# Kernel optimization log

Measured on AMD Instinct MI355X. Metric: run time of the kernel, lower is better.

## Reference

```python
import jax, jax.numpy as jnp
import numpy as np

B, D, H = 8192, 1024, 4096


def setup_inputs() -> dict:
    key = jax.random.key(0)
    ks = jax.random.split(key, 8)
    s_in = 1.0 / np.sqrt(D)
    s_hid = 1.0 / np.sqrt(H)
    return {
        "x": jax.random.normal(ks[0], (B, D), dtype=jnp.float32),
        "Wr": jax.random.normal(ks[1], (D, 1), dtype=jnp.float32) * s_in,
        "br": jnp.zeros((1,), dtype=jnp.float32),
        "W1l": jax.random.normal(ks[2], (D, H), dtype=jnp.float32) * s_in,
        "b1l": jnp.zeros((H,), dtype=jnp.float32),
        "W2l": jax.random.normal(ks[3], (H, D), dtype=jnp.float32) * s_hid,
        "b2l": jnp.zeros((D,), dtype=jnp.float32),
        "W1r": jax.random.normal(ks[4], (D, H), dtype=jnp.float32) * s_in,
        "b1r": jnp.zeros((H,), dtype=jnp.float32),
        "W2r": jax.random.normal(ks[5], (H, D), dtype=jnp.float32) * s_hid,
        "b2r": jnp.zeros((D,), dtype=jnp.float32),
    }


def _expert(x, W1, b1, W2, b2):
    # 2-layer MLP expert: [B, D] -> [B, H] -> [B, D]
    h = jax.nn.relu(x @ W1 + b1)
    return h @ W2 + b2


def reference(x, Wr, br, W1l, b1l, W2l, b2l, W1r, b1r, W2r, b2r):
    # Router probability p in (0, 1): [B, 1]
    p = jax.nn.sigmoid(x @ Wr + br)
    left = _expert(x, W1l, b1l, W2l, b2l)   # [B, D]
    right = _expert(x, W1r, b1r, W2r, b2r)  # [B, D]
    # soft_decision branch: convex combination of children per sample
    return p * left + (1.0 - p) * right
```

## Files before the change

### kernel.cpp

```cpp
#include <hip/hip_runtime.h>
#include <hip/hip_bf16.h>
#include <cstdint>
#include <cstddef>

#define B_DIM  8192
#define D_DIM  1024
#define H_DIM  4096
#define H2_DIM 8192

using bf16 = __hip_bfloat16;
typedef __attribute__((ext_vector_type(8))) short bf16x8;
typedef __attribute__((ext_vector_type(4))) float f32x4;

__global__ __launch_bounds__(256) void cast_f32_to_bf16(const float* __restrict__ in,
                                                        bf16* __restrict__ out, int n_vec8) {
    int i = blockIdx.x * 256 + threadIdx.x;
    if (i >= n_vec8) return;
    const float4* src = reinterpret_cast<const float4*>(in) + (size_t)i * 2;
    float4 a = src[0], b = src[1];
    union { bf16 h[8]; int4 u; } r;
    r.h[0] = __float2bfloat16(a.x); r.h[1] = __float2bfloat16(a.y);
    r.h[2] = __float2bfloat16(a.z); r.h[3] = __float2bfloat16(a.w);
    r.h[4] = __float2bfloat16(b.x); r.h[5] = __float2bfloat16(b.y);
    r.h[6] = __float2bfloat16(b.z); r.h[7] = __float2bfloat16(b.w);
    reinterpret_cast<int4*>(out)[i] = r.u;
}

__global__ __launch_bounds__(256) void router_kernel(const float* __restrict__ x,
                                                     const float* __restrict__ Wr,
                                                     const float* __restrict__ br,
                                                     float* __restrict__ p) {
    int wave = threadIdx.x >> 6, lane = threadIdx.x & 63;
    int row = blockIdx.x * 4 + wave;
    const float* xr = x + (size_t)row * D_DIM;
    float sum = 0.f;
#pragma unroll
    for (int it = 0; it < 4; ++it) {
        int k = it * 256 + lane * 4;
        float4 xv = *reinterpret_cast<const float4*>(xr + k);
        float4 wv = *reinterpret_cast<const float4*>(Wr + k);
        sum += xv.x * wv.x + xv.y * wv.y + xv.z * wv.z + xv.w * wv.w;
    }
#pragma unroll
    for (int off = 32; off >= 1; off >>= 1) sum += __shfl_down(sum, off, 64);
    if (lane == 0) p[row] = 1.f / (1.f + expf(-(sum + br[0])));
}

__global__ __launch_bounds__(256) void transpose_cast_kernel(const float* __restrict__ src,
                                                             int R, int C,
                                                             bf16* __restrict__ dst, int dstLD) {
    __shared__ float tile[32][33];
    int c0 = blockIdx.x * 32, r0 = blockIdx.y * 32;
    int tx = threadIdx.x & 31, ty = threadIdx.x >> 5;
#pragma unroll
    for (int i = 0; i < 32; i += 8)
        tile[ty + i][tx] = src[(size_t)(r0 + ty + i) * C + c0 + tx];
    __syncthreads();
#pragma unroll
    for (int i = 0; i < 32; i += 8)
        dst[(size_t)(c0 + ty + i) * dstLD + r0 + tx] = __float2bfloat16(tile[tx][ty + i]);
}

template<int NBH, int EPI>
__global__ __launch_bounds__(512, 2) void gemm8(const bf16* __restrict__ A,
                                                const bf16* __restrict__ Bt,
                                                void* __restrict__ Cout,
                                                int N, int K, int NT, int nbx,
                                                const float* __restrict__ p,
                                                const float* __restrict__ bias_l,
                                                const float* __restrict__ bias_r) {
    constexpr int NREP   = 2 * NBH;
    constexpr int HALF_B = 16384;
    constexpr int BUFB   = (2 + NBH) * HALF_B;
    constexpr int BN     = NBH * 128;
    __shared__ __align__(16) char lds[2 * BUFB];

    const int tid  = threadIdx.x;
    const int wid  = tid >> 6, lane = tid & 63;
    const int wr   = wid >> 2, wcn = wid & 3;

    const int cpx     = (int)gridDim.x >> 3;
    const int logical = ((int)blockIdx.x & 7) * cpx + ((int)blockIdx.x >> 3);
    const int by = logical / nbx, bx = logical - by * nbx;
    const int bm = by * 256, bn = bx * BN;

    const int      srow = tid >> 3;
    const uint32_t coff = (uint32_t)(((tid & 7) ^ (srow & 7)) << 3);
    uint32_t offA[2][2], offB[NBH][2];
#pragma unroll
    for (int h = 0; h < 2; ++h)
#pragma unroll
        for (int r = 0; r < 2; ++r)
            offA[h][r] = (uint32_t)(bm + h * 128 + r * 64 + srow) * (uint32_t)K + coff;
#pragma unroll
    for (int h = 0; h < NBH; ++h)
#pragma unroll
        for (int r = 0; r < 2; ++r)
            offB[h][r] = (uint32_t)(bn + h * 128 + r * 64 + srow) * (uint32_t)K + coff;

#define STAGE(PAR, KT) do {                                                                  \
    const uint32_t k64_ = (uint32_t)(KT) * 64u;                                              \
    _Pragma("unroll") for (int h_ = 0; h_ < 2; ++h_)                                         \
      _Pragma("unroll") for (int r_ = 0; r_ < 2; ++r_)                                       \
        __builtin_amdgcn_global_load_lds(                                                    \
          (const __attribute__((address_space(1))) uint32_t*)(A + (size_t)(offA[h_][r_] + k64_)), \
          (__attribute__((address_space(3))) uint32_t*)(lds + (PAR)*BUFB + h_*HALF_B + r_*8192 + wid*1024), \
          16, 0, 0);                                                                         \
    _Pragma("unroll") for (int h_ = 0; h_ < NBH; ++h_)                                       \
      _Pragma("unroll") for (int r_ = 0; r_ < 2; ++r_)                                       \
        __builtin_amdgcn_global_load_lds(                                                    \
          (const __attribute__((address_space(1))) uint32_t*)(Bt + (size_t)(offB[h_][r_] + k64_)), \
          (__attribute__((address_space(3))) uint32_t*)(lds + (PAR)*BUFB + (2+h_)*HALF_B + r_*8192 + wid*1024), \
          16, 0, 0);                                                                         \
} while (0)

    const int      lrow  = lane & 15, kg = lane >> 4;
    const uint32_t s0    = (uint32_t)((kg ^ (lrow & 7)) << 4);
    const uint32_t baseA = (uint32_t)(wr * HALF_B + lrow * 128) + s0;
    const int      colt0 = wcn * (NREP * 16);
    const uint32_t baseB = (uint32_t)((2 + (colt0 >> 7)) * HALF_B + ((colt0 & 127) + lrow) * 128) + s0;

#define RD(off) (*reinterpret_cast<const bf16x8*>(lds + (off)))

    f32x4 acc[8][NREP];
#pragma unroll
    for (int m = 0; m < 8; ++m)
#pragma unroll
        for (int n = 0; n < NREP; ++n) acc[m][n] = (f32x4){0.f, 0.f, 0.f, 0.f};

#define VM_WAIT_STEADY() do {                                              \
    if (NBH == 2) asm volatile("s_waitcnt vmcnt(8)" ::: "memory");         \
    else          asm volatile("s_waitcnt vmcnt(6)" ::: "memory");         \
} while (0)

#define TILE_BODY(PAR, KT, STG, LASTT) do {                                                   \
    bf16x8 bf_[NREP][2], af_[4][2];                                                           \
    _Pragma("unroll") for (int n = 0; n < NREP; ++n)                                          \
      _Pragma("unroll") for (int kk = 0; kk < 2; ++kk)                                        \
        bf_[n][kk] = RD(((uint32_t)((PAR)*BUFB) + baseB + (uint32_t)(n*2048)) ^ (uint32_t)(kk*64)); \
    _Pragma("unroll") for (int m = 0; m < 4; ++m)                                             \
      _Pragma("unroll") for (int kk = 0; kk < 2; ++kk)                                        \
        af_[m][kk] = RD(((uint32_t)((PAR)*BUFB) + baseA + (uint32_t)(m*2048)) ^ (uint32_t)(kk*64)); \
    __builtin_amdgcn_s_setprio(1);                                                            \
    _Pragma("unroll") for (int m = 0; m < 4; ++m)                                             \
      _Pragma("unroll") for (int n = 0; n < NREP; ++n)                                        \
        _Pragma("unroll") for (int kk = 0; kk < 2; ++kk)                                      \
          acc[m][n] = __builtin_amdgcn_mfma_f32_16x16x32_bf16(af_[m][kk], bf_[n][kk], acc[m][n], 0, 0, 0); \
    __builtin_amdgcn_s_setprio(0);                                                            \
    _Pragma("unroll") for (int m = 0; m < 4; ++m)                                             \
      _Pragma("unroll") for (int kk = 0; kk < 2; ++kk)                                        \
        af_[m][kk] = RD(((uint32_t)((PAR)*BUFB) + baseA + (uint32_t)(8192 + m*2048)) ^ (uint32_t)(kk*64)); \
    __builtin_amdgcn_sched_barrier(0);                                                        \
    asm volatile("s_waitcnt lgkmcnt(0)" ::: "memory");                                        \
    __builtin_amdgcn_sched_barrier(0);                                                        \
    __builtin_amdgcn_s_barrier();                                                             \
    __builtin_amdgcn_sched_barrier(0);                                                        \
    if (STG) { STAGE(PAR, (KT) + 2); }                                                        \
    __builtin_amdgcn_sched_barrier(0);                                                        \
    __builtin_amdgcn_s_setprio(1);                                                            \
    _Pragma("unroll") for (int m = 0; m < 4; ++m)                                             \
      _Pragma("unroll") for (int n = 0; n < NREP; ++n)                                        \
        _Pragma("unroll") for (int kk = 0; kk < 2; ++kk)                                      \
          acc[4+m][n] = __builtin_amdgcn_mfma_f32_16x16x32_bf16(af_[m][kk], bf_[n][kk], acc[4+m][n], 0, 0, 0); \
    __builtin_amdgcn_s_setprio(0);                                                            \
    if (!(LASTT)) {                                                                           \
      __builtin_amdgcn_sched_barrier(0);                                                      \
      if (STG) { VM_WAIT_STEADY(); }                                                          \
      else     { asm volatile("s_waitcnt vmcnt(0)" ::: "memory"); }                           \
      __builtin_amdgcn_sched_barrier(0);                                                      \
      __builtin_amdgcn_s_barrier();                                                           \
      __builtin_amdgcn_sched_barrier(0);                                                      \
    }                                                                                         \
} while (0)

    STAGE(0, 0);
    STAGE(1, 1);
    VM_WAIT_STEADY();
    __builtin_amdgcn_sched_barrier(0);
    __builtin_amdgcn_s_barrier();
    __builtin_amdgcn_sched_barrier(0);

    int kt = 0;
    for (; kt < NT - 2; kt += 2) {
        TILE_BODY(0, kt,     true, false);
        TILE_BODY(1, kt + 1, true, false);
    }
    TILE_BODY(0, NT - 2, false, false);
    TILE_BODY(1, NT - 1, false, true);

    const int crow0 = bm + wr * 128 + (kg << 2);
    const int ccol0 = bn + wcn * (NREP * 16) + lrow;

    if (EPI == 1) {
        bf16* __restrict__ Ho = (bf16*)Cout;
#pragma unroll
        for (int n = 0; n < NREP; ++n) {
            const int col = ccol0 + n * 16;
            const bool left = col < H_DIM;
            const float bias = left ? bias_l[col] : bias_r[col - H_DIM];
#pragma unroll
            for (int m = 0; m < 8; ++m) {
#pragma unroll
                for (int j = 0; j < 4; ++j) {
                    const int row = crow0 + m * 16 + j;
                    const float pw = p[row];
                    const float scale = left ? pw : 1.f - pw;
                    const float v = fmaxf(acc[m][n][j] + bias, 0.f) * scale;
                    Ho[(size_t)row * N + col] = __float2bfloat16(v);
                }
            }
        }
    } else {
        float* __restrict__ Co = (float*)Cout;
#pragma unroll
        for (int n = 0; n < NREP; ++n) {
            const int col = ccol0 + n * 16;
            const float bl = bias_l[col];
            const float brr = bias_r[col];
#pragma unroll
            for (int m = 0; m < 8; ++m) {
#pragma unroll
                for (int j = 0; j < 4; ++j) {
                    const int row = crow0 + m * 16 + j;
                    const float pw = p[row];
                    Co[(size_t)row * N + col] = acc[m][n][j] + pw * bl + (1.f - pw) * brr;
                }
            }
        }
    }
#undef TILE_BODY
#undef VM_WAIT_STEADY
#undef RD
#undef STAGE
}

extern "C" void kernel_launch(void* const* d_in, const int* in_sizes, int n_in,
                              void* d_out, int out_size, void* d_ws, size_t ws_size,
                              hipStream_t stream) {
    const float* x   = (const float*)d_in[0];
    const float* Wr  = (const float*)d_in[1];
    const float* br  = (const float*)d_in[2];
    const float* W1l = (const float*)d_in[3];
    const float* b1l = (const float*)d_in[4];
    const float* W2l = (const float*)d_in[5];
    const float* b2l = (const float*)d_in[6];
    const float* W1r = (const float*)d_in[7];
    const float* b1r = (const float*)d_in[8];
    const float* W2r = (const float*)d_in[9];
    const float* b2r = (const float*)d_in[10];
    float* out = (float*)d_out;

    char* ws = (char*)d_ws;
    bf16*  x_bf = (bf16*)(ws);
    bf16*  W1t  = (bf16*)(ws + (size_t)(16u << 20));
    bf16*  hbuf = (bf16*)(ws + (size_t)(32u << 20));
    float* pbuf = (float*)(ws + (size_t)(160u << 20));
    bf16*  W2t  = x_bf;

    cast_f32_to_bf16<<<(B_DIM * D_DIM / 8 + 255) / 256, 256, 0, stream>>>(x, x_bf, B_DIM * D_DIM / 8);
    router_kernel<<<B_DIM / 4, 256, 0, stream>>>(x, Wr, br, pbuf);

    transpose_cast_kernel<<<dim3(H_DIM / 32, D_DIM / 32), 256, 0, stream>>>(W1l, D_DIM, H_DIM, W1t, D_DIM);
    transpose_cast_kernel<<<dim3(H_DIM / 32, D_DIM / 32), 256, 0, stream>>>(W1r, D_DIM, H_DIM,
                                                                            W1t + (size_t)H_DIM * D_DIM, D_DIM);
    gemm8<2, 1><<<1024, 512, 0, stream>>>(x_bf, W1t, hbuf, H2_DIM, D_DIM, D_DIM / 64, 32,
                                          pbuf, b1l, b1r);

    transpose_cast_kernel<<<dim3(D_DIM / 32, H_DIM / 32), 256, 0, stream>>>(W2l, H_DIM, D_DIM, W2t, H2_DIM);
    transpose_cast_kernel<<<dim3(D_DIM / 32, H_DIM / 32), 256, 0, stream>>>(W2r, H_DIM, D_DIM, W2t + H_DIM, H2_DIM);

    gemm8<1, 0><<<256, 512, 0, stream>>>(hbuf, W2t, out, D_DIM, H2_DIM, H2_DIM / 64, 8,
                                         pbuf, b2l, b2r);
}
```

Before: 457.5 us.

## Restructure GEMM main loop into fine-grained phases interleaving loads with MFMA

Rewrites the GEMM k-loop so each double-buffered tile is split into phases (2 or 4 per tile, depending on NBH). Each phase reads an A sub-slice, issues one slice of the global-to-LDS prefetch, and runs its MFMAs. Prefetch of the next A and B tiles is spread across these phases instead of being issued in one burst, and the vmcnt waits are retuned to match. The aim is smoother overlap of memory traffic with MFMA work, at the cost of more barriers per tile and more complex buffer-reuse ordering.

```diff
diff --git a/kernel.cpp b/kernel.cpp
--- a/kernel.cpp
+++ b/kernel.cpp
@@ -69,10 +69,11 @@
                                                 const float* __restrict__ p,
                                                 const float* __restrict__ bias_l,
                                                 const float* __restrict__ bias_r) {
-    constexpr int NREP   = 2 * NBH;
-    constexpr int HALF_B = 16384;
-    constexpr int BUFB   = (2 + NBH) * HALF_B;
-    constexpr int BN     = NBH * 128;
+    constexpr int NREP  = 2 * NBH;
+    constexpr int MPP   = (NBH == 2) ? 2 : 4;
+    constexpr int HALF  = 16384;
+    constexpr int NHALF = 2 + NBH;
+    constexpr int BUFB  = NHALF * HALF;
     __shared__ __align__(16) char lds[2 * BUFB];
 
     const int tid  = threadIdx.x;
@@ -82,114 +83,132 @@
     const int cpx     = (int)gridDim.x >> 3;
     const int logical = ((int)blockIdx.x & 7) * cpx + ((int)blockIdx.x >> 3);
     const int by = logical / nbx, bx = logical - by * nbx;
-    const int bm = by * 256, bn = bx * BN;
-
-    const int      srow = tid >> 3;
-    const uint32_t coff = (uint32_t)(((tid & 7) ^ (srow & 7)) << 3);
-    uint32_t offA[2][2], offB[NBH][2];
-#pragma unroll
-    for (int h = 0; h < 2; ++h)
-#pragma unroll
-        for (int r = 0; r < 2; ++r)
-            offA[h][r] = (uint32_t)(bm + h * 128 + r * 64 + srow) * (uint32_t)K + coff;
-#pragma unroll
-    for (int h = 0; h < NBH; ++h)
-#pragma unroll
-        for (int r = 0; r < 2; ++r)
-            offB[h][r] = (uint32_t)(bn + h * 128 + r * 64 + srow) * (uint32_t)K + coff;
-
-#define STAGE(PAR, KT) do {                                                                  \
-    const uint32_t k64_ = (uint32_t)(KT) * 64u;                                              \
-    _Pragma("unroll") for (int h_ = 0; h_ < 2; ++h_)                                         \
-      _Pragma("unroll") for (int r_ = 0; r_ < 2; ++r_)                                       \
-        __builtin_amdgcn_global_load_lds(                                                    \
-          (const __attribute__((address_space(1))) uint32_t*)(A + (size_t)(offA[h_][r_] + k64_)), \
-          (__attribute__((address_space(3))) uint32_t*)(lds + (PAR)*BUFB + h_*HALF_B + r_*8192 + wid*1024), \
-          16, 0, 0);                                                                         \
-    _Pragma("unroll") for (int h_ = 0; h_ < NBH; ++h_)                                       \
-      _Pragma("unroll") for (int r_ = 0; r_ < 2; ++r_)                                       \
-        __builtin_amdgcn_global_load_lds(                                                    \
-          (const __attribute__((address_space(1))) uint32_t*)(Bt + (size_t)(offB[h_][r_] + k64_)), \
-          (__attribute__((address_space(3))) uint32_t*)(lds + (PAR)*BUFB + (2+h_)*HALF_B + r_*8192 + wid*1024), \
-          16, 0, 0);                                                                         \
-} while (0)
-
-    const int      lrow  = lane & 15, kg = lane >> 4;
-    const uint32_t s0    = (uint32_t)((kg ^ (lrow & 7)) << 4);
-    const uint32_t baseA = (uint32_t)(wr * HALF_B + lrow * 128) + s0;
+    const int bm = by * 256, bn = bx * (NBH * 128);
+
+    const int      r0   = tid >> 3;
+    const uint32_t cswz = (uint32_t)(((tid & 7) ^ (r0 & 7)) << 3);
+    uint32_t offA[2], offB[NBH];
+#pragma unroll
+    for (int h = 0; h < 2; ++h)    offA[h] = (uint32_t)(bm + h * 128 + r0) * (uint32_t)K + cswz;
+#pragma unroll
+    for (int h = 0; h < NBH; ++h)  offB[h] = (uint32_t)(bn + h * 128 + r0) * (uint32_t)K + cswz;
+
+#define STGH(G, P, HI, EOFF) do {                                                             \
+    _Pragma("unroll") for (int j_ = 0; j_ < 2; ++j_)                                          \
+        __builtin_amdgcn_global_load_lds(                                                     \
+            (const __attribute__((address_space(1))) uint32_t*)((G) + (size_t)(EOFF) + (size_t)(j_ * 64) * (size_t)K), \
+            (__attribute__((address_space(3))) uint32_t*)(lds + (P) * BUFB + (HI) * HALF + j_ * 8192 + wid * 1024), \
+            16, 0, 0);                                                                        \
+} while (0)
+
+    const int      lrow = lane & 15, kg8 = lane >> 4;
+    const uint32_t swz  = (uint32_t)((kg8 ^ (lrow & 7)) << 4);
+    const uint32_t sAb  = (uint32_t)(wr * HALF) + (uint32_t)(lrow * 128) + swz;
     const int      colt0 = wcn * (NREP * 16);
-    const uint32_t baseB = (uint32_t)((2 + (colt0 >> 7)) * HALF_B + ((colt0 & 127) + lrow) * 128) + s0;
-
-#define RD(off) (*reinterpret_cast<const bf16x8*>(lds + (off)))
-
+    const uint32_t sBb  = (uint32_t)((2 + (colt0 >> 7)) * HALF) + (uint32_t)(((colt0 & 127) + lrow) * 128) + swz;
+
+#define RD(o) (*reinterpret_cast<const bf16x8*>(lds + (o)))
+
+    bf16x8 bf[NREP][2];
+    bf16x8 af[MPP][2];
     f32x4 acc[8][NREP];
 #pragma unroll
     for (int m = 0; m < 8; ++m)
 #pragma unroll
         for (int n = 0; n < NREP; ++n) acc[m][n] = (f32x4){0.f, 0.f, 0.f, 0.f};
 
-#define VM_WAIT_STEADY() do {                                              \
-    if (NBH == 2) asm volatile("s_waitcnt vmcnt(8)" ::: "memory");         \
-    else          asm volatile("s_waitcnt vmcnt(6)" ::: "memory");         \
-} while (0)
-
-#define TILE_BODY(PAR, KT, STG, LASTT) do {                                                   \
-    bf16x8 bf_[NREP][2], af_[4][2];                                                           \
-    _Pragma("unroll") for (int n = 0; n < NREP; ++n)                                          \
-      _Pragma("unroll") for (int kk = 0; kk < 2; ++kk)                                        \
-        bf_[n][kk] = RD(((uint32_t)((PAR)*BUFB) + baseB + (uint32_t)(n*2048)) ^ (uint32_t)(kk*64)); \
-    _Pragma("unroll") for (int m = 0; m < 4; ++m)                                             \
-      _Pragma("unroll") for (int kk = 0; kk < 2; ++kk)                                        \
-        af_[m][kk] = RD(((uint32_t)((PAR)*BUFB) + baseA + (uint32_t)(m*2048)) ^ (uint32_t)(kk*64)); \
-    __builtin_amdgcn_s_setprio(1);                                                            \
-    _Pragma("unroll") for (int m = 0; m < 4; ++m)                                             \
-      _Pragma("unroll") for (int n = 0; n < NREP; ++n)                                        \
-        _Pragma("unroll") for (int kk = 0; kk < 2; ++kk)                                      \
-          acc[m][n] = __builtin_amdgcn_mfma_f32_16x16x32_bf16(af_[m][kk], bf_[n][kk], acc[m][n], 0, 0, 0); \
-    __builtin_amdgcn_s_setprio(0);                                                            \
-    _Pragma("unroll") for (int m = 0; m < 4; ++m)                                             \
-      _Pragma("unroll") for (int kk = 0; kk < 2; ++kk)                                        \
-        af_[m][kk] = RD(((uint32_t)((PAR)*BUFB) + baseA + (uint32_t)(8192 + m*2048)) ^ (uint32_t)(kk*64)); \
-    __builtin_amdgcn_sched_barrier(0);                                                        \
+#define RDBF(P) do {                                                                          \
+    _Pragma("unroll") for (int n_ = 0; n_ < NREP; ++n_)                                       \
+      _Pragma("unroll") for (int k_ = 0; k_ < 2; ++k_)                                        \
+        bf[n_][k_] = RD((uint32_t)((P) * BUFB) + ((sBb + (uint32_t)(n_ * 2048)) ^ (uint32_t)(k_ << 6))); \
+} while (0)
+
+#define RDAF(P, M0) do {                                                                      \
+    _Pragma("unroll") for (int m_ = 0; m_ < MPP; ++m_)                                        \
+      _Pragma("unroll") for (int k_ = 0; k_ < 2; ++k_)                                        \
+        af[m_][k_] = RD((uint32_t)((P) * BUFB) + ((sAb + (uint32_t)((((M0) + m_) * 2048))) ^ (uint32_t)(k_ << 6))); \
+} while (0)
+
+#define MFMAQ(M0) do {                                                                        \
+    _Pragma("unroll") for (int m_ = 0; m_ < MPP; ++m_)                                        \
+      _Pragma("unroll") for (int n_ = 0; n_ < NREP; ++n_)                                     \
+        _Pragma("unroll") for (int k_ = 0; k_ < 2; ++k_)                                      \
+          acc[(M0) + m_][n_] = __builtin_amdgcn_mfma_f32_16x16x32_bf16(af[m_][k_], bf[n_][k_], acc[(M0) + m_][n_], 0, 0, 0); \
+} while (0)
+
+#define VMC(NSTR) do { asm volatile("s_waitcnt vmcnt(" NSTR ")" ::: "memory");                \
+                       __builtin_amdgcn_sched_barrier(0); } while (0)
+
+#define PH(P, M0, FIRSTP, STAGES, WAITS, TRAILB) do {                                         \
+    if (FIRSTP) RDBF(P);                                                                      \
+    RDAF(P, M0);                                                                              \
+    STAGES                                                                                    \
+    __builtin_amdgcn_s_barrier();                                                             \
     asm volatile("s_waitcnt lgkmcnt(0)" ::: "memory");                                        \
     __builtin_amdgcn_sched_barrier(0);                                                        \
-    __builtin_amdgcn_s_barrier();                                                             \
+    __builtin_amdgcn_s_setprio(1);                                                            \
+    MFMAQ(M0);                                                                                \
+    __builtin_amdgcn_s_setprio(0);                                                            \
     __builtin_amdgcn_sched_barrier(0);                                                        \
-    if (STG) { STAGE(PAR, (KT) + 2); }                                                        \
-    __builtin_amdgcn_sched_barrier(0);                                                        \
-    __builtin_amdgcn_s_setprio(1);                                                            \
-    _Pragma("unroll") for (int m = 0; m < 4; ++m)                                             \
-      _Pragma("unroll") for (int n = 0; n < NREP; ++n)                                        \
-        _Pragma("unroll") for (int kk = 0; kk < 2; ++kk)                                      \
-          acc[4+m][n] = __builtin_amdgcn_mfma_f32_16x16x32_bf16(af_[m][kk], bf_[n][kk], acc[4+m][n], 0, 0, 0); \
-    __builtin_amdgcn_s_setprio(0);                                                            \
-    if (!(LASTT)) {                                                                           \
-      __builtin_amdgcn_sched_barrier(0);                                                      \
-      if (STG) { VM_WAIT_STEADY(); }                                                          \
-      else     { asm volatile("s_waitcnt vmcnt(0)" ::: "memory"); }                           \
-      __builtin_amdgcn_sched_barrier(0);                                                      \
-      __builtin_amdgcn_s_barrier();                                                           \
-      __builtin_amdgcn_sched_barrier(0);                                                      \
-    }                                                                                         \
-} while (0)
-
-    STAGE(0, 0);
-    STAGE(1, 1);
-    VM_WAIT_STEADY();
-    __builtin_amdgcn_sched_barrier(0);
+    WAITS                                                                                     \
+    if (TRAILB) { __builtin_amdgcn_s_barrier(); __builtin_amdgcn_sched_barrier(0); }          \
+} while (0)
+
+    if constexpr (NBH == 2) {
+        STGH(A, 0, 0, offA[0]); STGH(A, 0, 1, offA[1]);
+        STGH(Bt, 0, 2, offB[0]); STGH(Bt, 0, 3, offB[1]);
+        STGH(Bt, 1, 2, offB[0] + 64); STGH(Bt, 1, 3, offB[1] + 64);
+        VMC("4");
+    } else {
+        STGH(A, 0, 0, offA[0]); STGH(A, 0, 1, offA[1]); STGH(Bt, 0, 2, offB[0]);
+        STGH(Bt, 1, 2, offB[0] + 64);
+        VMC("2");
+    }
     __builtin_amdgcn_s_barrier();
     __builtin_amdgcn_sched_barrier(0);
 
-    int kt = 0;
-    for (; kt < NT - 2; kt += 2) {
-        TILE_BODY(0, kt,     true, false);
-        TILE_BODY(1, kt + 1, true, false);
-    }
-    TILE_BODY(0, NT - 2, false, false);
-    TILE_BODY(1, NT - 1, false, true);
-
-    const int crow0 = bm + wr * 128 + (kg << 2);
-    const int ccol0 = bn + wcn * (NREP * 16) + lrow;
+    const int NIT = NT >> 1;
+    for (int i = 0; i < NIT - 1; ++i) {
+        const uint32_t k1 = (uint32_t)(2 * i + 1) * 64u;
+        const uint32_t k2 = (uint32_t)(2 * i + 2) * 64u;
+        const uint32_t k3 = (uint32_t)(2 * i + 3) * 64u;
+        if constexpr (NBH == 2) {
+            PH(0, 0, true,  { STGH(A, 1, 0, offA[0] + k1); }, , true);
+            PH(0, 2, false, { STGH(A, 1, 1, offA[1] + k1); }, , true);
+            PH(0, 4, false, { STGH(Bt, 0, 2, offB[0] + k2); }, , true);
+            PH(0, 6, false, { STGH(Bt, 0, 3, offB[1] + k2); }, VMC("4");, true);
+            PH(1, 0, true,  { STGH(A, 0, 0, offA[0] + k2); }, , true);
+            PH(1, 2, false, { STGH(A, 0, 1, offA[1] + k2); }, , true);
+            PH(1, 4, false, { STGH(Bt, 1, 2, offB[0] + k3); }, , true);
+            PH(1, 6, false, { STGH(Bt, 1, 3, offB[1] + k3); }, VMC("4");, true);
+        } else {
+            PH(0, 0, true,  { STGH(A, 1, 0, offA[0] + k1); STGH(A, 1, 1, offA[1] + k1); }, , true);
+            PH(0, 4, false, { STGH(Bt, 0, 2, offB[0] + k2); }, VMC("2");, true);
+            PH(1, 0, true,  { STGH(A, 0, 0, offA[0] + k2); STGH(A, 0, 1, offA[1] + k2); }, , true);
+            PH(1, 4, false, { STGH(Bt, 1, 2, offB[0] + k3); }, VMC("2");, true);
+        }
+    }
+    {
+        const uint32_t kl = (uint32_t)(NT - 1) * 64u;
+        if constexpr (NBH == 2) {
+            PH(0, 0, true,  { STGH(A, 1, 0, offA[0] + kl); }, , true);
+            PH(0, 2, false, { STGH(A, 1, 1, offA[1] + kl); }, , true);
+            PH(0, 4, false, , , true);
+            PH(0, 6, false, , VMC("0");, true);
+            PH(1, 0, true,  , , true);
+            PH(1, 2, false, , , true);
+            PH(1, 4, false, , , true);
+            PH(1, 6, false, , , false);
+        } else {
+            PH(0, 0, true,  { STGH(A, 1, 0, offA[0] + kl); STGH(A, 1, 1, offA[1] + kl); }, , true);
+            PH(0, 4, false, , VMC("0");, true);
+            PH(1, 0, true,  , , true);
+            PH(1, 4, false, , , false);
+        }
+    }
+
+    const int crow0 = bm + wr * 128 + (kg8 << 2);
+    const int ccol0 = bn + colt0 + lrow;
 
     if (EPI == 1) {
         bf16* __restrict__ Ho = (bf16*)Cout;
@@ -228,10 +247,13 @@
             }
         }
     }
-#undef TILE_BODY
-#undef VM_WAIT_STEADY
+#undef PH
+#undef VMC
+#undef MFMAQ
+#undef RDAF
+#undef RDBF
 #undef RD
-#undef STAGE
+#undef STGH
 }
 
 extern "C" void kernel_launch(void* const* d_in, const int* in_sizes, int n_in,
```

Measured after the change: 461.9 us. Within noise of the previous version (+0.9%).
